# Optimization experiments

Hardware: AMD Instinct MI355X
Metric: run time of the kernel (lower is better)

Reference implementation:

```python
import jax, jax.numpy as jnp
import numpy as np

NA, NF, EA, EF, NG = 200000, 50000, 800000, 200000, 4096
D = 128
BN_EPS = 1e-5

def _bn(x, g, b):
    m = x.mean(axis=0)
    v = x.var(axis=0)
    return g * (x - m) * jax.lax.rsqrt(v + BN_EPS) + b

def _gine(x, src, dst, edge_emb, W1, b1, g1, be1, W2, b2):
    # message = relu(x_src + edge_emb); scatter-add to dst; (1+eps)*x with eps=0
    msg = jax.nn.relu(x[src] + edge_emb)
    agg = jax.ops.segment_sum(msg, dst, num_segments=x.shape[0])
    h = x + agg
    h = jax.nn.relu(_bn(h @ W1 + b1, g1, be1))
    return h @ W2 + b2

def _seg_mean(x, idx, n):
    s = jax.ops.segment_sum(x, idx, num_segments=n)
    c = jax.ops.segment_sum(jnp.ones((x.shape[0],), x.dtype), idx, num_segments=n)
    return s / jnp.maximum(c, 1.0)[:, None]

def setup_inputs() -> dict:
    key = jax.random.key(0)
    ks = jax.random.split(key, 40)
    def nrm(i, shape, scale=0.05):
        return (jax.random.normal(ks[i], shape, dtype=jnp.float32) * scale)
    inp = {
        'atom_x': jax.random.normal(ks[0], (NA, 101), dtype=jnp.float32),
        'fg_x': jax.random.normal(ks[1], (NF, 73), dtype=jnp.float32),
        'atom_edge_attr': jax.random.normal(ks[2], (EA, 11), dtype=jnp.float32),
        'fg_edge_attr': jax.random.normal(ks[3], (EF, 101), dtype=jnp.float32),
        'atom_emb_W': nrm(4, (101, D)), 'atom_emb_b': jnp.zeros((D,), jnp.float32),
        'fg_emb_W': nrm(5, (73, D)), 'fg_emb_b': jnp.zeros((D,), jnp.float32),
        'bond_W': nrm(6, (3, 11, D)), 'bond_b': jnp.zeros((3, D), jnp.float32),
        'ag_W1': nrm(7, (3, D, 2 * D)), 'ag_b1': jnp.zeros((3, 2 * D), jnp.float32),
        'ag_g1': jnp.ones((3, 2 * D), jnp.float32), 'ag_be1': jnp.zeros((3, 2 * D), jnp.float32),
        'ag_W2': nrm(8, (3, 2 * D, D)), 'ag_b2': jnp.zeros((3, D), jnp.float32),
        'abn_g': jnp.ones((3, D), jnp.float32), 'abn_b': jnp.zeros((3, D), jnp.float32),
        'fge_W': nrm(9, (2, 101, D)), 'fge_b': jnp.zeros((2, D), jnp.float32),
        'fg_W1': nrm(10, (2, D, 2 * D)), 'fg_b1': jnp.zeros((2, 2 * D), jnp.float32),
        'fg_g1': jnp.ones((2, 2 * D), jnp.float32), 'fg_be1': jnp.zeros((2, 2 * D), jnp.float32),
        'fg_W2': nrm(11, (2, 2 * D, D)), 'fg_b2': jnp.zeros((2, D), jnp.float32),
        'fbn_g': jnp.ones((2, D), jnp.float32), 'fbn_b': jnp.zeros((2, D), jnp.float32),
        'a2f_W': nrm(12, (D, D)), 'a2f_b': jnp.zeros((D,), jnp.float32),
        'atom_edge_index': jax.random.randint(ks[13], (2, EA), 0, NA, dtype=jnp.int32),
        'fg_edge_index': jax.random.randint(ks[14], (2, EF), 0, NF, dtype=jnp.int32),
        'atom_idx': jax.random.randint(ks[15], (NA,), 0, NA, dtype=jnp.int32),
        'fg_idx': jax.random.randint(ks[16], (NA,), 0, NF, dtype=jnp.int32),
        'fg_batch': jnp.sort(jax.random.randint(ks[17], (NF,), 0, NG, dtype=jnp.int32)),
    }
    return inp

def reference(atom_x, fg_x, atom_edge_attr, fg_edge_attr, atom_emb_W, atom_emb_b, fg_emb_W, fg_emb_b, bond_W, bond_b, ag_W1, ag_b1, ag_g1, ag_be1, ag_W2, ag_b2, abn_g, abn_b, fge_W, fge_b, fg_W1, fg_b1, fg_g1, fg_be1, fg_W2, fg_b2, fbn_g, fbn_b, a2f_W, a2f_b, atom_edge_index, fg_edge_index, atom_idx, fg_idx, fg_batch):
    asrc, adst = atom_edge_index[0], atom_edge_index[1]
    fsrc, fdst = fg_edge_index[0], fg_edge_index[1]
    h = atom_x @ atom_emb_W + atom_emb_b
    for i in range(3):
        eemb = atom_edge_attr @ bond_W[i] + bond_b[i]
        h = _gine(h, asrc, adst, eemb, ag_W1[i], ag_b1[i], ag_g1[i], ag_be1[i], ag_W2[i], ag_b2[i])
        h = _bn(h, abn_g[i], abn_b[i])
        if i != 2:
            h = jax.nn.relu(h)
    a2f = _seg_mean(h[atom_idx], fg_idx, NF) @ a2f_W + a2f_b
    g = fg_x @ fg_emb_W + fg_emb_b + a2f
    for i in range(2):
        eemb = fg_edge_attr @ fge_W[i] + fge_b[i]
        g = _gine(g, fsrc, fdst, eemb, fg_W1[i], fg_b1[i], fg_g1[i], fg_be1[i], fg_W2[i], fg_b2[i])
        g = _bn(g, fbn_g[i], fbn_b[i])
        if i != 1:
            g = jax.nn.relu(g)
    return _seg_mean(g, fg_batch, NG)
```

## Files before the change

### kernel.cpp

```cpp
#include <hip/hip_runtime.h>
#include <cstddef>
#include <cstdint>

#define NA_C 200000
#define NF_C 50000
#define EA_C 800000
#define EF_C 200000
#define NG_C 4096
#define DD 128
#define HH 256
#define SC_CHUNK 2048

typedef unsigned short u16;
typedef unsigned int   u32;
typedef float f32x4 __attribute__((ext_vector_type(4)));
typedef short s16x8 __attribute__((ext_vector_type(8)));

__device__ inline float bf2f(u16 h) { return __uint_as_float(((u32)h) << 16); }
__device__ inline u16 f2bf(float f) {
    u32 u = __float_as_uint(f);
    return (u16)((u + 0x7fffu + ((u >> 16) & 1u)) >> 16);
}
__device__ inline float2 up2(u32 u) {
    return make_float2(__uint_as_float(u << 16), __uint_as_float(u & 0xffff0000u));
}
__device__ inline u32 pk2(float x, float y) { return (u32)f2bf(x) | ((u32)f2bf(y) << 16); }

__global__ __launch_bounds__(256) void gemm_b(
    const u16* __restrict__ A, const u16* __restrict__ Bt,
    const float* __restrict__ bias,
    const float* __restrict__ iscale, const float* __restrict__ ishift,
    const u16* __restrict__ Cadd, u16* __restrict__ C,
    int M, int K, int Ntot,
    float* __restrict__ ssum, float* __restrict__ ssq)
{
    __shared__ u16 As[4 * 128 * 8];
    __shared__ u16 Bs[4 * 128 * 8];
    __shared__ float ls[128], lq[128];
    const int tid  = threadIdx.x;
    const int wave = tid >> 6, lane = tid & 63;
    const int quad = lane >> 4, l15 = lane & 15;
    const int wm = (wave & 1) * 64, wn = (wave >> 1) * 64;
    const int m0 = blockIdx.y * 128, n0 = blockIdx.x * 128;
    const int r     = tid >> 1;
    const int cpair = (tid & 1) * 2;

    f32x4 acc[4][4];
#pragma unroll
    for (int i = 0; i < 4; ++i)
#pragma unroll
        for (int j = 0; j < 4; ++j) acc[i][j] = (f32x4)0.f;

    const int m = m0 + r;
    for (int k0 = 0; k0 < K; k0 += 32) {
#pragma unroll
        for (int j = 0; j < 2; ++j) {
            const int cg = cpair + j;
            uint4 av = make_uint4(0, 0, 0, 0);
            if (m < M) av = *(const uint4*)(A + (size_t)m * K + k0 + cg * 8);
            if (iscale) {
                u32* w = (u32*)&av;
#pragma unroll
                for (int q2 = 0; q2 < 4; ++q2) {
                    int kk = k0 + cg * 8 + q2 * 2;
                    float2 f = up2(w[q2]);
                    f.x = fmaxf(fmaf(f.x, iscale[kk],     ishift[kk]),     0.f);
                    f.y = fmaxf(fmaf(f.y, iscale[kk + 1], ishift[kk + 1]), 0.f);
                    w[q2] = pk2(f.x, f.y);
                }
            }
            *(uint4*)&As[(cg * 128 + r) * 8] = av;
        }
#pragma unroll
        for (int j = 0; j < 2; ++j) {
            const int cg = cpair + j;
            uint4 bv = *(const uint4*)(Bt + (size_t)(n0 + r) * K + k0 + cg * 8);
            *(uint4*)&Bs[(cg * 128 + r) * 8] = bv;
        }
        __syncthreads();

        s16x8 a[4], b[4];
#pragma unroll
        for (int mi = 0; mi < 4; ++mi)
            a[mi] = *(const s16x8*)&As[(quad * 128 + wm + mi * 16 + l15) * 8];
#pragma unroll
        for (int ni = 0; ni < 4; ++ni)
            b[ni] = *(const s16x8*)&Bs[(quad * 128 + wn + ni * 16 + l15) * 8];
#pragma unroll
        for (int mi = 0; mi < 4; ++mi)
#pragma unroll
            for (int ni = 0; ni < 4; ++ni)
                acc[mi][ni] = __builtin_amdgcn_mfma_f32_16x16x32_bf16(
                    a[mi], b[ni], acc[mi][ni], 0, 0, 0);
        __syncthreads();
    }

    if (ssum) {
        if (tid < 128) { ls[tid] = 0.f; lq[tid] = 0.f; }
        __syncthreads();
    }

    float cs[4] = {0.f, 0.f, 0.f, 0.f}, cq[4] = {0.f, 0.f, 0.f, 0.f};
#pragma unroll
    for (int mi = 0; mi < 4; ++mi) {
        int rowb = m0 + wm + mi * 16 + quad * 4;
#pragma unroll
        for (int ni = 0; ni < 4; ++ni) {
            int col = n0 + wn + ni * 16 + l15;
            float bv = bias[col];
#pragma unroll
            for (int rr = 0; rr < 4; ++rr) {
                int row = rowb + rr;
                if (row < M) {
                    float v = acc[mi][ni][rr] + bv;
                    size_t idx = (size_t)row * Ntot + col;
                    if (Cadd) v += bf2f(Cadd[idx]);
                    C[idx] = f2bf(v);
                    cs[ni] += v;
                    cq[ni] = fmaf(v, v, cq[ni]);
                }
            }
        }
    }

    if (ssum) {
#pragma unroll
        for (int ni = 0; ni < 4; ++ni) {
            int lc = wn + ni * 16 + l15;
            atomicAdd(&ls[lc], cs[ni]);
            atomicAdd(&lq[lc], cq[ni]);
        }
        __syncthreads();
        if (tid < 128) {
            atomicAdd(&ssum[n0 + tid], ls[tid]);
            atomicAdd(&ssq[n0 + tid], lq[tid]);
        }
    }
}

static inline void gemm_launch(hipStream_t s, const u16* A, const u16* Bt,
    const float* bias, const float* iscale, const float* ishift,
    const u16* Cadd, u16* C, int M, int K, int Ntot,
    float* ssum = nullptr, float* ssq = nullptr)
{
    dim3 grid(Ntot / 128, (M + 127) / 128);
    gemm_b<<<grid, dim3(256), 0, s>>>(A, Bt, bias, iscale, ishift, Cadd, C,
                                      M, K, Ntot, ssum, ssq);
}

__global__ void cvt_pad(const float* __restrict__ src, u32* __restrict__ dst,
                        int M, int K, int Kp2)
{
    int idx = blockIdx.x * 256 + threadIdx.x;
    if (idx >= M * Kp2) return;
    int row = idx / Kp2, c = (idx - row * Kp2) * 2;
    float a = (c < K)     ? src[(size_t)row * K + c]     : 0.f;
    float b = (c + 1 < K) ? src[(size_t)row * K + c + 1] : 0.f;
    dst[idx] = pk2(a, b);
}

__global__ void prep_wt(const float* __restrict__ W, u16* __restrict__ Wt,
                        int K, int N, int Kp)
{
    int idx = blockIdx.x * 256 + threadIdx.x;
    if (idx >= N * Kp) return;
    int n = idx / Kp, k = idx - n * Kp;
    Wt[idx] = (k < K) ? f2bf(W[(size_t)k * N + n]) : (u16)0;
}

__global__ void hist_k(const int* __restrict__ idx, int n, int* __restrict__ deg)
{
    int i = blockIdx.x * 256 + threadIdx.x;
    if (i < n) atomicAdd(&deg[idx[i]], 1);
}

__global__ __launch_bounds__(256) void scan_part_k(const int* __restrict__ deg, int n,
                                                   int* __restrict__ bsum)
{
    __shared__ int ts[256];
    const int t = threadIdx.x;
    const int base = blockIdx.x * SC_CHUNK + t * 8;
    int s = 0;
#pragma unroll
    for (int j = 0; j < 8; ++j) { int i = base + j; if (i < n) s += deg[i]; }
    ts[t] = s;
    __syncthreads();
    for (int off = 128; off > 0; off >>= 1) {
        if (t < off) ts[t] += ts[t + off];
        __syncthreads();
    }
    if (t == 0) bsum[blockIdx.x] = ts[0];
}

__global__ __launch_bounds__(256) void scan_top_k(int* __restrict__ bsum, int nb)
{
    __shared__ int ss[256];
    const int t = threadIdx.x;
    int v = (t < nb) ? bsum[t] : 0;
    ss[t] = v;
    __syncthreads();
    for (int off = 1; off < 256; off <<= 1) {
        int u = (t >= off) ? ss[t - off] : 0;
        __syncthreads();
        ss[t] += u;
        __syncthreads();
    }
    if (t < nb) bsum[t] = ss[t] - v;
}

__global__ __launch_bounds__(256) void scan_emit_k(const int* __restrict__ deg, int n,
                                                   const int* __restrict__ bsum,
                                                   int* __restrict__ rowptr)
{
    __shared__ int ts[256];
    const int t = threadIdx.x;
    const int base = blockIdx.x * SC_CHUNK + t * 8;
    int d[8], loc[8], s = 0;
#pragma unroll
    for (int j = 0; j < 8; ++j) {
        int i = base + j;
        d[j] = (i < n) ? deg[i] : 0;
        loc[j] = s;
        s += d[j];
    }
    ts[t] = s;
    __syncthreads();
    for (int off = 1; off < 256; off <<= 1) {
        int u = (t >= off) ? ts[t - off] : 0;
        __syncthreads();
        ts[t] += u;
        __syncthreads();
    }
    const int off0 = bsum[blockIdx.x] + (ts[t] - s);
#pragma unroll
    for (int j = 0; j < 8; ++j) {
        int i = base + j;
        if (i < n) {
            rowptr[i] = off0 + loc[j];
            if (i == n - 1) rowptr[n] = off0 + loc[j] + d[j];
        }
    }
}

static void csr_prefix(hipStream_t s, const int* idx, int ne, int nbkt,
                       int* rowptr, int* cursor, int* bsum)
{
    hipMemsetAsync(cursor, 0, (size_t)nbkt * 4, s);
    hist_k<<<(ne + 255) / 256, 256, 0, s>>>(idx, ne, cursor);
    int nblk = (nbkt + SC_CHUNK - 1) / SC_CHUNK;
    scan_part_k<<<nblk, 256, 0, s>>>(cursor, nbkt, bsum);
    scan_top_k<<<1, 256, 0, s>>>(bsum, nblk);
    scan_emit_k<<<nblk, 256, 0, s>>>(cursor, nbkt, bsum, rowptr);
    hipMemcpyAsync(cursor, rowptr, (size_t)nbkt * 4, hipMemcpyDeviceToDevice, s);
}

__global__ void fill2_k(const int* __restrict__ idx, const int* __restrict__ src,
                        int n, int* __restrict__ cursor, int2* __restrict__ csr2)
{
    int i = blockIdx.x * 256 + threadIdx.x;
    if (i < n) {
        int p = atomicAdd(&cursor[idx[i]], 1);
        csr2[p] = make_int2(i, src[i]);
    }
}

__global__ void fillm_k(const int* __restrict__ idx, const int* __restrict__ map,
                        int n, int* __restrict__ cursor, int* __restrict__ csr)
{
    int i = blockIdx.x * 256 + threadIdx.x;
    if (i < n) {
        int p = atomicAdd(&cursor[idx[i]], 1);
        csr[p] = map ? map[i] : i;
    }
}

__global__ __launch_bounds__(256) void gine_agg_atom_b(
    const u32* __restrict__ x2, const float* __restrict__ attr,
    const int2* __restrict__ csr2, const int* __restrict__ rowptr,
    const float* __restrict__ Wm, const float* __restrict__ bm,
    const float* __restrict__ tsc, const float* __restrict__ tsh, int trelu,
    u32* __restrict__ out2, int n)
{
    __shared__ float2 sW[11][64];
    __shared__ float2 sb[64];
    for (int i = threadIdx.x; i < 11 * 64; i += 256) {
        int k = i >> 6, l = i & 63;
        sW[k][l] = make_float2(Wm[k * 128 + 2 * l], Wm[k * 128 + 2 * l + 1]);
    }
    if (threadIdx.x < 64)
        sb[threadIdx.x] = make_float2(bm[2 * threadIdx.x], bm[2 * threadIdx.x + 1]);
    __syncthreads();
    const int lane = threadIdx.x & 63;
    const int v = blockIdx.x * 4 + (threadIdx.x >> 6);
    if (v >= n) return;
    float sc0 = 1.f, sc1 = 1.f, sh0 = 0.f, sh1 = 0.f;
    if (tsc) {
        sc0 = tsc[2 * lane]; sc1 = tsc[2 * lane + 1];
        sh0 = tsh[2 * lane]; sh1 = tsh[2 * lane + 1];
    }
    float2 xv = up2(x2[(size_t)v * 64 + lane]);
    xv.x = fmaf(xv.x, sc0, sh0); xv.y = fmaf(xv.y, sc1, sh1);
    if (trelu) { xv.x = fmaxf(xv.x, 0.f); xv.y = fmaxf(xv.y, 0.f); }
    float2 acc = xv;
    const int e1 = rowptr[v + 1];
    for (int e = rowptr[v]; e < e1; ++e) {
        int2 p = csr2[e];
        const float* ar = attr + (size_t)p.x * 11;
        float m0 = sb[lane].x, m1 = sb[lane].y;
#pragma unroll
        for (int k = 0; k < 11; ++k) {
            float a = ar[k];
            m0 = fmaf(a, sW[k][lane].x, m0);
            m1 = fmaf(a, sW[k][lane].y, m1);
        }
        float2 s = up2(x2[(size_t)p.y * 64 + lane]);
        s.x = fmaf(s.x, sc0, sh0); s.y = fmaf(s.y, sc1, sh1);
        if (trelu) { s.x = fmaxf(s.x, 0.f); s.y = fmaxf(s.y, 0.f); }
        acc.x += fmaxf(s.x + m0, 0.f);
        acc.y += fmaxf(s.y + m1, 0.f);
    }
    out2[(size_t)v * 64 + lane] = pk2(acc.x, acc.y);
}

__global__ __launch_bounds__(256) void gine_agg_pre_b(
    const u32* __restrict__ x2, const u32* __restrict__ eemb2,
    const int2* __restrict__ csr2, const int* __restrict__ rowptr,
    const float* __restrict__ tsc, const float* __restrict__ tsh, int trelu,
    u32* __restrict__ out2, int n)
{
    const int lane = threadIdx.x & 63;
    const int v = blockIdx.x * 4 + (threadIdx.x >> 6);
    if (v >= n) return;
    float sc0 = 1.f, sc1 = 1.f, sh0 = 0.f, sh1 = 0.f;
    if (tsc) {
        sc0 = tsc[2 * lane]; sc1 = tsc[2 * lane + 1];
        sh0 = tsh[2 * lane]; sh1 = tsh[2 * lane + 1];
    }
    float2 xv = up2(x2[(size_t)v * 64 + lane]);
    xv.x = fmaf(xv.x, sc0, sh0); xv.y = fmaf(xv.y, sc1, sh1);
    if (trelu) { xv.x = fmaxf(xv.x, 0.f); xv.y = fmaxf(xv.y, 0.f); }
    float2 acc = xv;
    const int e1 = rowptr[v + 1];
    for (int e = rowptr[v]; e < e1; ++e) {
        int2 p = csr2[e];
        float2 m = up2(eemb2[(size_t)p.x * 64 + lane]);
        float2 s = up2(x2[(size_t)p.y * 64 + lane]);
        s.x = fmaf(s.x, sc0, sh0); s.y = fmaf(s.y, sc1, sh1);
        if (trelu) { s.x = fmaxf(s.x, 0.f); s.y = fmaxf(s.y, 0.f); }
        acc.x += fmaxf(m.x + s.x, 0.f);
        acc.y += fmaxf(m.y + s.y, 0.f);
    }
    out2[(size_t)v * 64 + lane] = pk2(acc.x, acc.y);
}

__global__ __launch_bounds__(256) void seg_mean_b2b(
    const u32* __restrict__ x2, const int* __restrict__ csr,
    const int* __restrict__ rowptr,
    const float* __restrict__ tsc, const float* __restrict__ tsh,
    u32* __restrict__ out2, int n)
{
    const int lane = threadIdx.x & 63;
    const int v = blockIdx.x * 4 + (threadIdx.x >> 6);
    if (v >= n) return;
    const int e0 = rowptr[v], e1 = rowptr[v + 1];
    float2 acc = make_float2(0.f, 0.f);
    for (int e = e0; e < e1; ++e) {
        float2 s = up2(x2[(size_t)csr[e] * 64 + lane]);
        acc.x += s.x; acc.y += s.y;
    }
    float inv = 1.f / fmaxf((float)(e1 - e0), 1.f);
    float2 r = make_float2(acc.x * inv, acc.y * inv);
    if (tsc) {
        if (e1 > e0) {
            r.x = fmaf(r.x, tsc[2 * lane],     tsh[2 * lane]);
            r.y = fmaf(r.y, tsc[2 * lane + 1], tsh[2 * lane + 1]);
        } else {
            r.x = 0.f; r.y = 0.f;
        }
    }
    out2[(size_t)v * 64 + lane] = pk2(r.x, r.y);
}

__global__ __launch_bounds__(256) void seg_mean_b2f(
    const u32* __restrict__ x2, const int* __restrict__ csr,
    const int* __restrict__ rowptr,
    const float* __restrict__ tsc, const float* __restrict__ tsh,
    float* __restrict__ out, int n)
{
    const int lane = threadIdx.x & 63;
    const int v = blockIdx.x * 4 + (threadIdx.x >> 6);
    if (v >= n) return;
    const int e0 = rowptr[v], e1 = rowptr[v + 1];
    float2 acc = make_float2(0.f, 0.f);
    for (int e = e0; e < e1; ++e) {
        float2 s = up2(x2[(size_t)csr[e] * 64 + lane]);
        acc.x += s.x; acc.y += s.y;
    }
    float inv = 1.f / fmaxf((float)(e1 - e0), 1.f);
    float2 r = make_float2(acc.x * inv, acc.y * inv);
    if (tsc) {
        if (e1 > e0) {
            r.x = fmaf(r.x, tsc[2 * lane],     tsh[2 * lane]);
            r.y = fmaf(r.y, tsc[2 * lane + 1], tsh[2 * lane + 1]);
        } else {
            r.x = 0.f; r.y = 0.f;
        }
    }
    *(float2*)&out[(size_t)v * 128 + lane * 2] = r;
}

__global__ void bn_finalize(const float* __restrict__ sum, const float* __restrict__ sumsq,
                            const float* __restrict__ g, const float* __restrict__ be,
                            float minv, float* __restrict__ sc, float* __restrict__ sh, int N)
{
    int c = threadIdx.x;
    if (c < N) {
        float m = sum[c] * minv;
        float v = fmaxf(sumsq[c] * minv - m * m, 0.f);
        float s = g[c] * rsqrtf(v + 1e-5f);
        sc[c] = s;
        sh[c] = fmaf(-m, s, be[c]);
    }
}

extern "C" void kernel_launch(void* const* d_in, const int* in_sizes, int n_in,
                              void* d_out, int out_size, void* d_ws, size_t ws_size,
                              hipStream_t stream)
{
    const float* atom_x        = (const float*)d_in[0];
    const float* fg_x          = (const float*)d_in[1];
    const float* atom_edge_attr= (const float*)d_in[2];
    const float* fg_edge_attr  = (const float*)d_in[3];
    const float* atom_emb_W    = (const float*)d_in[4];
    const float* atom_emb_b    = (const float*)d_in[5];
    const float* fg_emb_W      = (const float*)d_in[6];
    const float* fg_emb_b      = (const float*)d_in[7];
    const float* bond_W        = (const float*)d_in[8];
    const float* bond_b        = (const float*)d_in[9];
    const float* ag_W1         = (const float*)d_in[10];
    const float* ag_b1         = (const float*)d_in[11];
    const float* ag_g1         = (const float*)d_in[12];
    const float* ag_be1        = (const float*)d_in[13];
    const float* ag_W2         = (const float*)d_in[14];
    const float* ag_b2         = (const float*)d_in[15];
    const float* abn_g         = (const float*)d_in[16];
    const float* abn_b         = (const float*)d_in[17];
    const float* fge_W         = (const float*)d_in[18];
    const float* fge_b         = (const float*)d_in[19];
    const float* fg_W1         = (const float*)d_in[20];
    const float* fg_b1         = (const float*)d_in[21];
    const float* fg_g1         = (const float*)d_in[22];
    const float* fg_be1        = (const float*)d_in[23];
    const float* fg_W2         = (const float*)d_in[24];
    const float* fg_b2         = (const float*)d_in[25];
    const float* fbn_g         = (const float*)d_in[26];
    const float* fbn_b         = (const float*)d_in[27];
    const float* a2f_W         = (const float*)d_in[28];
    const float* a2f_b         = (const float*)d_in[29];
    const int*   aei           = (const int*)d_in[30];
    const int*   fei           = (const int*)d_in[31];
    const int*   atom_idx      = (const int*)d_in[32];
    const int*   fg_idx       = (const int*)d_in[33];
    const int*   fg_batch      = (const int*)d_in[34];
    const int *asrc = aei, *adst = aei + EA_C;
    const int *fsrc = fei, *fdst = fei + EF_C;

    char* base = (char*)d_ws;
    const size_t SZ_H = (size_t)NA_C * DD * 2;
    u16* hA = (u16*)base;
    u16* hB = (u16*)(base + SZ_H);
    u16* TB = (u16*)(base + 2 * SZ_H);
    u16* XB = (u16*)(base + 2 * SZ_H + (size_t)NA_C * HH * 2);
    char* csrb = (char*)XB + SZ_H;
    int*  aR  = (int*)csrb;
    int*  aCu = aR + (NA_C + 2);
    int*  bS  = aCu + NA_C;
    int2* aE2 = (int2*)(bS + 258);
    char* wtb = (char*)(aE2 + EA_C);
    wtb = (char*)(((uintptr_t)wtb + 15) & ~(uintptr_t)15);
    u16* WT_aemb = (u16*)wtb;                 wtb += 128 * 128 * 2;
    u16* WT_aW1  = (u16*)wtb;                 wtb += 3 * 256 * 128 * 2;
    u16* WT_aW2  = (u16*)wtb;                 wtb += 3 * 128 * 256 * 2;
    u16* WT_a2f  = (u16*)wtb;                 wtb += 128 * 128 * 2;
    u16* WT_femb = (u16*)wtb;                 wtb += 128 * 96 * 2;
    u16* WT_fge  = (u16*)wtb;                 wtb += 2 * 128 * 128 * 2;
    u16* WT_fW1  = (u16*)wtb;                 wtb += 2 * 256 * 128 * 2;
    u16* WT_fW2  = (u16*)wtb;                 wtb += 2 * 128 * 256 * 2;
    float* sm    = (float*)wtb;               wtb += 1024 * sizeof(float);
    float* s_sum = sm;
    float* s_sq  = sm + 256;
    float* s_sc  = sm + 512;
    float* s_sh  = sm + 768;

    {
        int g = (128 * 128 + 255) / 256;
        prep_wt<<<g, 256, 0, stream>>>(atom_emb_W, WT_aemb, 101, 128, 128);
        prep_wt<<<g, 256, 0, stream>>>(a2f_W, WT_a2f, 128, 128, 128);
        for (int i = 0; i < 3; ++i) {
            prep_wt<<<(256 * 128 + 255) / 256, 256, 0, stream>>>(
                ag_W1 + (size_t)i * 128 * 256, WT_aW1 + (size_t)i * 256 * 128, 128, 256, 128);
            prep_wt<<<(128 * 256 + 255) / 256, 256, 0, stream>>>(
                ag_W2 + (size_t)i * 256 * 128, WT_aW2 + (size_t)i * 128 * 256, 256, 128, 256);
        }
        prep_wt<<<(128 * 96 + 255) / 256, 256, 0, stream>>>(fg_emb_W, WT_femb, 73, 128, 96);
        for (int i = 0; i < 2; ++i) {
            prep_wt<<<g, 256, 0, stream>>>(
                fge_W + (size_t)i * 101 * 128, WT_fge + (size_t)i * 128 * 128, 101, 128, 128);
            prep_wt<<<(256 * 128 + 255) / 256, 256, 0, stream>>>(
                fg_W1 + (size_t)i * 128 * 256, WT_fW1 + (size_t)i * 256 * 128, 128, 256, 128);
            prep_wt<<<(128 * 256 + 255) / 256, 256, 0, stream>>>(
                fg_W2 + (size_t)i * 256 * 128, WT_fW2 + (size_t)i * 128 * 256, 256, 128, 256);
        }
    }

    csr_prefix(stream, adst, EA_C, NA_C, aR, aCu, bS);
    fill2_k<<<(EA_C + 255) / 256, 256, 0, stream>>>(adst, asrc, EA_C, aCu, aE2);

    cvt_pad<<<((size_t)NA_C * 64 + 255) / 256, 256, 0, stream>>>(atom_x, (u32*)XB, NA_C, 101, 64);

    gemm_launch(stream, XB, WT_aemb, atom_emb_b, nullptr, nullptr, nullptr, hA, NA_C, 128, 128);

    u16* hc = hA;
    const float* cur_sc = nullptr;
    const float* cur_sh = nullptr;
    int cur_relu = 0;
    for (int i = 0; i < 3; ++i) {
        u16* hn = (hc == hA) ? hB : hA;
        gine_agg_atom_b<<<(NA_C + 3) / 4, 256, 0, stream>>>(
            (const u32*)hc, atom_edge_attr, aE2, aR,
            bond_W + (size_t)i * 11 * DD, bond_b + i * DD,
            cur_sc, cur_sh, cur_relu, (u32*)hn, NA_C);
        hipMemsetAsync(s_sum, 0, 512 * sizeof(float), stream);
        gemm_launch(stream, hn, WT_aW1 + (size_t)i * 256 * 128,
                    ag_b1 + i * HH, nullptr, nullptr, nullptr, TB, NA_C, 128, HH,
                    s_sum, s_sq);
        bn_finalize<<<1, HH, 0, stream>>>(s_sum, s_sq, ag_g1 + i * HH, ag_be1 + i * HH,
                                          1.f / NA_C, s_sc, s_sh, HH);
        hipMemsetAsync(s_sum, 0, 512 * sizeof(float), stream);
        gemm_launch(stream, TB, WT_aW2 + (size_t)i * 128 * 256,
                    ag_b2 + i * DD, s_sc, s_sh, nullptr, hn, NA_C, 256, 128,
                    s_sum, s_sq);
        bn_finalize<<<1, DD, 0, stream>>>(s_sum, s_sq, abn_g + i * DD, abn_b + i * DD,
                                          1.f / NA_C, s_sc, s_sh, DD);
        cur_sc = s_sc; cur_sh = s_sh; cur_relu = (i != 2);
        hc = hn;
    }

    {
        int* xE = (int*)aE2;
        csr_prefix(stream, fg_idx, NA_C, NF_C, aR, aCu, bS);
        fillm_k<<<(NA_C + 255) / 256, 256, 0, stream>>>(fg_idx, atom_idx, NA_C, aCu, xE);
        seg_mean_b2b<<<(NF_C + 3) / 4, 256, 0, stream>>>(
            (const u32*)hc, xE, aR, s_sc, s_sh, (u32*)hA, NF_C);
    }
    u16* means   = hA;
    u16* a2f_lin = hA + (size_t)NF_C * DD;
    gemm_launch(stream, means, WT_a2f, a2f_b, nullptr, nullptr, nullptr, a2f_lin, NF_C, 128, 128);

    u16* fgx_bf = hA + (size_t)NF_C * DD * 2;
    cvt_pad<<<((size_t)NF_C * 48 + 255) / 256, 256, 0, stream>>>(fg_x, (u32*)fgx_bf, NF_C, 73, 48);
    u16* g = hB;
    gemm_launch(stream, fgx_bf, WT_femb, fg_emb_b, nullptr, nullptr, a2f_lin, g, NF_C, 96, 128);

    cvt_pad<<<((size_t)EF_C * 64 + 255) / 256, 256, 0, stream>>>(fg_edge_attr, (u32*)XB, EF_C, 101, 64);
    csr_prefix(stream, fdst, EF_C, NF_C, aR, aCu, bS);
    fill2_k<<<(EF_C + 255) / 256, 256, 0, stream>>>(fdst, fsrc, EF_C, aCu, aE2);

    u16* eemb = TB;
    u16* gn   = hA + (size_t)NF_C * DD * 2 + (size_t)NF_C * 96;
    u16* gt   = TB + (size_t)EF_C * DD;
    const float* gsc = nullptr;
    const float* gsh = nullptr;
    int grelu = 0;
    for (int i = 0; i < 2; ++i) {
        gemm_launch(stream, XB, WT_fge + (size_t)i * 128 * 128,
                    fge_b + i * DD, nullptr, nullptr, nullptr, eemb, EF_C, 128, 128);
        gine_agg_pre_b<<<(NF_C + 3) / 4, 256, 0, stream>>>(
            (const u32*)g, (const u32*)eemb, aE2, aR, gsc, gsh, grelu, (u32*)gn, NF_C);
        hipMemsetAsync(s_sum, 0, 512 * sizeof(float), stream);
        gemm_launch(stream, gn, WT_fW1 + (size_t)i * 256 * 128,
                    fg_b1 + i * HH, nullptr, nullptr, nullptr, gt, NF_C, 128, HH,
                    s_sum, s_sq);
        bn_finalize<<<1, HH, 0, stream>>>(s_sum, s_sq, fg_g1 + i * HH, fg_be1 + i * HH,
                                          1.f / NF_C, s_sc, s_sh, HH);
        hipMemsetAsync(s_sum, 0, 512 * sizeof(float), stream);
        gemm_launch(stream, gt, WT_fW2 + (size_t)i * 128 * 256,
                    fg_b2 + i * DD, s_sc, s_sh, nullptr, g, NF_C, 256, 128,
                    s_sum, s_sq);
        bn_finalize<<<1, DD, 0, stream>>>(s_sum, s_sq, fbn_g + i * DD, fbn_b + i * DD,
                                          1.f / NF_C, s_sc, s_sh, DD);
        gsc = s_sc; gsh = s_sh; grelu = (i != 1);
    }

    {
        int* bR  = (int*)(gt + (size_t)NF_C * HH);
        int* bCu = bR + (NG_C + 1);
        int* bE  = bCu + NG_C;
        csr_prefix(stream, fg_batch, NF_C, NG_C, bR, bCu, bS);
        fillm_k<<<(NF_C + 255) / 256, 256, 0, stream>>>(fg_batch, nullptr, NF_C, bCu, bE);
        seg_mean_b2f<<<(NG_C + 3) / 4, 256, 0, stream>>>(
            (const u32*)g, bE, bR, s_sc, s_sh, (float*)d_out, NG_C);
    }
}
```

Baseline: 2.229 ms.

## Permute edge attributes into CSR order and software-pipeline gather loops

Edge attributes for the atom and functional-group graphs are reordered once into destination-sorted CSR order. Atom attrs are padded to 12 floats so they load as three float4 values, and the fg edge-embedding GEMM input is permuted the same way. Aggregation kernels then read edge data contiguously instead of through a random gather. They also prefetch the next edge's source row, attributes and embedding, which overlaps load latency with compute. The cost is an extra permutation pass over the 800k atom edges and a few more registers in the aggregation loops.

```diff
diff --git a/kernel.cpp b/kernel.cpp
--- a/kernel.cpp
+++ b/kernel.cpp
@@ -159,6 +159,28 @@
     dst[idx] = pk2(a, b);
 }
 
+__global__ void cvt_pad_perm(const float* __restrict__ src, const int2* __restrict__ csr2,
+                             u32* __restrict__ dst, int M, int K, int Kp2)
+{
+    int idx = blockIdx.x * 256 + threadIdx.x;
+    if (idx >= M * Kp2) return;
+    int row = idx / Kp2, c = (idx - row * Kp2) * 2;
+    int srow = csr2[row].x;
+    float a = (c < K)     ? src[(size_t)srow * K + c]     : 0.f;
+    float b = (c + 1 < K) ? src[(size_t)srow * K + c + 1] : 0.f;
+    dst[idx] = pk2(a, b);
+}
+
+__global__ void perm_attr12_k(const float* __restrict__ attr, const int2* __restrict__ csr2,
+                              float* __restrict__ out, int ne)
+{
+    int idx = blockIdx.x * 256 + threadIdx.x;
+    if (idx >= ne * 12) return;
+    int e = idx / 12, k = idx - e * 12;
+    int eid = csr2[e].x;
+    out[idx] = (k < 11) ? attr[(size_t)eid * 11 + k] : 0.f;
+}
+
 __global__ void prep_wt(const float* __restrict__ W, u16* __restrict__ Wt,
                         int K, int N, int Kp)
 {
@@ -275,7 +297,7 @@
 }
 
 __global__ __launch_bounds__(256) void gine_agg_atom_b(
-    const u32* __restrict__ x2, const float* __restrict__ attr,
+    const u32* __restrict__ x2, const float4* __restrict__ attrp,
     const int2* __restrict__ csr2, const int* __restrict__ rowptr,
     const float* __restrict__ Wm, const float* __restrict__ bm,
     const float* __restrict__ tsc, const float* __restrict__ tsh, int trelu,
@@ -302,22 +324,35 @@
     xv.x = fmaf(xv.x, sc0, sh0); xv.y = fmaf(xv.y, sc1, sh1);
     if (trelu) { xv.x = fmaxf(xv.x, 0.f); xv.y = fmaxf(xv.y, 0.f); }
     float2 acc = xv;
-    const int e1 = rowptr[v + 1];
-    for (int e = rowptr[v]; e < e1; ++e) {
-        int2 p = csr2[e];
-        const float* ar = attr + (size_t)p.x * 11;
-        float m0 = sb[lane].x, m1 = sb[lane].y;
-#pragma unroll
-        for (int k = 0; k < 11; ++k) {
-            float a = ar[k];
-            m0 = fmaf(a, sW[k][lane].x, m0);
-            m1 = fmaf(a, sW[k][lane].y, m1);
-        }
-        float2 s = up2(x2[(size_t)p.y * 64 + lane]);
-        s.x = fmaf(s.x, sc0, sh0); s.y = fmaf(s.y, sc1, sh1);
-        if (trelu) { s.x = fmaxf(s.x, 0.f); s.y = fmaxf(s.y, 0.f); }
-        acc.x += fmaxf(s.x + m0, 0.f);
-        acc.y += fmaxf(s.y + m1, 0.f);
+    const int e0 = rowptr[v], e1 = rowptr[v + 1];
+    if (e0 < e1) {
+        int2  pc = csr2[e0];
+        float4 a0c = attrp[3 * (size_t)e0];
+        float4 a1c = attrp[3 * (size_t)e0 + 1];
+        float4 a2c = attrp[3 * (size_t)e0 + 2];
+        u32   xc = x2[(size_t)pc.y * 64 + lane];
+        for (int e = e0; e < e1; ++e) {
+            const int en = (e + 1 < e1) ? e + 1 : e;
+            int2  pn = csr2[en];
+            float4 a0n = attrp[3 * (size_t)en];
+            float4 a1n = attrp[3 * (size_t)en + 1];
+            float4 a2n = attrp[3 * (size_t)en + 2];
+            u32   xn = x2[(size_t)pn.y * 64 + lane];
+            float ar[12];
+            *(float4*)&ar[0] = a0c; *(float4*)&ar[4] = a1c; *(float4*)&ar[8] = a2c;
+            float m0 = sb[lane].x, m1 = sb[lane].y;
+#pragma unroll
+            for (int k = 0; k < 11; ++k) {
+                m0 = fmaf(ar[k], sW[k][lane].x, m0);
+                m1 = fmaf(ar[k], sW[k][lane].y, m1);
+            }
+            float2 s = up2(xc);
+            s.x = fmaf(s.x, sc0, sh0); s.y = fmaf(s.y, sc1, sh1);
+            if (trelu) { s.x = fmaxf(s.x, 0.f); s.y = fmaxf(s.y, 0.f); }
+            acc.x += fmaxf(s.x + m0, 0.f);
+            acc.y += fmaxf(s.y + m1, 0.f);
+            pc = pn; a0c = a0n; a1c = a1n; a2c = a2n; xc = xn;
+        }
     }
     out2[(size_t)v * 64 + lane] = pk2(acc.x, acc.y);
 }
@@ -340,15 +375,24 @@
     xv.x = fmaf(xv.x, sc0, sh0); xv.y = fmaf(xv.y, sc1, sh1);
     if (trelu) { xv.x = fmaxf(xv.x, 0.f); xv.y = fmaxf(xv.y, 0.f); }
     float2 acc = xv;
-    const int e1 = rowptr[v + 1];
-    for (int e = rowptr[v]; e < e1; ++e) {
-        int2 p = csr2[e];
-        float2 m = up2(eemb2[(size_t)p.x * 64 + lane]);
-        float2 s = up2(x2[(size_t)p.y * 64 + lane]);
-        s.x = fmaf(s.x, sc0, sh0); s.y = fmaf(s.y, sc1, sh1);
-        if (trelu) { s.x = fmaxf(s.x, 0.f); s.y = fmaxf(s.y, 0.f); }
-        acc.x += fmaxf(m.x + s.x, 0.f);
-        acc.y += fmaxf(m.y + s.y, 0.f);
+    const int e0 = rowptr[v], e1 = rowptr[v + 1];
+    if (e0 < e1) {
+        int2 pc = csr2[e0];
+        u32  xc = x2[(size_t)pc.y * 64 + lane];
+        u32  mc = eemb2[(size_t)e0 * 64 + lane];
+        for (int e = e0; e < e1; ++e) {
+            const int en = (e + 1 < e1) ? e + 1 : e;
+            int2 pn = csr2[en];
+            u32  xn = x2[(size_t)pn.y * 64 + lane];
+            u32  mn = eemb2[(size_t)en * 64 + lane];
+            float2 m = up2(mc);
+            float2 s = up2(xc);
+            s.x = fmaf(s.x, sc0, sh0); s.y = fmaf(s.y, sc1, sh1);
+            if (trelu) { s.x = fmaxf(s.x, 0.f); s.y = fmaxf(s.y, 0.f); }
+            acc.x += fmaxf(m.x + s.x, 0.f);
+            acc.y += fmaxf(m.y + s.y, 0.f);
+            pc = pn; xc = xn; mc = mn;
+        }
     }
     out2[(size_t)v * 64 + lane] = pk2(acc.x, acc.y);
 }
@@ -364,9 +408,15 @@
     if (v >= n) return;
     const int e0 = rowptr[v], e1 = rowptr[v + 1];
     float2 acc = make_float2(0.f, 0.f);
-    for (int e = e0; e < e1; ++e) {
-        float2 s = up2(x2[(size_t)csr[e] * 64 + lane]);
-        acc.x += s.x; acc.y += s.y;
+    if (e0 < e1) {
+        u32 xc = x2[(size_t)csr[e0] * 64 + lane];
+        for (int e = e0; e < e1; ++e) {
+            const int en = (e + 1 < e1) ? e + 1 : e;
+            u32 xn = x2[(size_t)csr[en] * 64 + lane];
+            float2 s = up2(xc);
+            acc.x += s.x; acc.y += s.y;
+            xc = xn;
+        }
     }
     float inv = 1.f / fmaxf((float)(e1 - e0), 1.f);
     float2 r = make_float2(acc.x * inv, acc.y * inv);
@@ -392,9 +442,15 @@
     if (v >= n) return;
     const int e0 = rowptr[v], e1 = rowptr[v + 1];
     float2 acc = make_float2(0.f, 0.f);
-    for (int e = e0; e < e1; ++e) {
-        float2 s = up2(x2[(size_t)csr[e] * 64 + lane]);
-        acc.x += s.x; acc.y += s.y;
+    if (e0 < e1) {
+        u32 xc = x2[(size_t)csr[e0] * 64 + lane];
+        for (int e = e0; e < e1; ++e) {
+            const int en = (e + 1 < e1) ? e + 1 : e;
+            u32 xn = x2[(size_t)csr[en] * 64 + lane];
+            float2 s = up2(xc);
+            acc.x += s.x; acc.y += s.y;
+            xc = xn;
+        }
     }
     float inv = 1.f / fmaxf((float)(e1 - e0), 1.f);
     float2 r = make_float2(acc.x * inv, acc.y * inv);
@@ -460,7 +516,7 @@
     const int*   aei           = (const int*)d_in[30];
     const int*   fei           = (const int*)d_in[31];
     const int*   atom_idx      = (const int*)d_in[32];
-    const int*   fg_idx       = (const int*)d_in[33];
+    const int*   fg_idx        = (const int*)d_in[33];
     const int*   fg_batch      = (const int*)d_in[34];
     const int *asrc = aei, *adst = aei + EA_C;
     const int *fsrc = fei, *fdst = fei + EF_C;
@@ -520,6 +576,10 @@
 
     gemm_launch(stream, XB, WT_aemb, atom_emb_b, nullptr, nullptr, nullptr, hA, NA_C, 128, 128);
 
+    float* attrP = (float*)XB;
+    perm_attr12_k<<<((size_t)EA_C * 12 + 255) / 256, 256, 0, stream>>>(
+        atom_edge_attr, aE2, attrP, EA_C);
+
     u16* hc = hA;
     const float* cur_sc = nullptr;
     const float* cur_sh = nullptr;
@@ -527,7 +587,7 @@
     for (int i = 0; i < 3; ++i) {
         u16* hn = (hc == hA) ? hB : hA;
         gine_agg_atom_b<<<(NA_C + 3) / 4, 256, 0, stream>>>(
-            (const u32*)hc, atom_edge_attr, aE2, aR,
+            (const u32*)hc, (const float4*)attrP, aE2, aR,
             bond_W + (size_t)i * 11 * DD, bond_b + i * DD,
             cur_sc, cur_sh, cur_relu, (u32*)hn, NA_C);
         hipMemsetAsync(s_sum, 0, 512 * sizeof(float), stream);
@@ -562,9 +622,10 @@
     u16* g = hB;
     gemm_launch(stream, fgx_bf, WT_femb, fg_emb_b, nullptr, nullptr, a2f_lin, g, NF_C, 96, 128);
 
-    cvt_pad<<<((size_t)EF_C * 64 + 255) / 256, 256, 0, stream>>>(fg_edge_attr, (u32*)XB, EF_C, 101, 64);
     csr_prefix(stream, fdst, EF_C, NF_C, aR, aCu, bS);
     fill2_k<<<(EF_C + 255) / 256, 256, 0, stream>>>(fdst, fsrc, EF_C, aCu, aE2);
+    cvt_pad_perm<<<((size_t)EF_C * 64 + 255) / 256, 256, 0, stream>>>(
+        fg_edge_attr, aE2, (u32*)XB, EF_C, 101, 64);
 
     u16* eemb = TB;
     u16* gn   = hA + (size_t)NF_C * DD * 2 + (size_t)NF_C * 96;
```

New measurement: 2.178 ms. 1.02x faster.
